# Kernel tuning notes

Measured on AMD Instinct MI355X. Metric: run time of the kernel, lower is better.

Reference implementation:

```python
import jax, jax.numpy as jnp
import numpy as np

NUM_CLASSES = 81
THRESH_HI = 0.5
THRESH_LO = 0.4
GAMMA = 2.0
ALPHA = 0.25
VARIANCE = (0.1, 0.2)  # cfg['variance'] in ssd.pytorch
B, P, T = 32, 24564, 20


def setup_inputs() -> dict:
    key = jax.random.key(0)
    k1, k2, k3, k4, k5, k6, k7 = jax.random.split(key, 7)
    loc_data = jax.random.normal(k1, (B, P, 4), jnp.float32)
    conf_data = jax.random.normal(k2, (B, P, NUM_CLASSES), jnp.float32)
    # priors in center form (cx, cy, w, h), all in [0,1]
    pcxy = jax.random.uniform(k3, (P, 2), minval=0.05, maxval=0.95)
    pwh = jax.random.uniform(k4, (P, 2), minval=0.04, maxval=0.5)
    priors = jnp.concatenate([pcxy, pwh], axis=-1).astype(jnp.float32)
    # ground-truth boxes in point form (xmin, ymin, xmax, ymax) + label
    tcxy = jax.random.uniform(k5, (B, T, 2), minval=0.1, maxval=0.9)
    twh = jax.random.uniform(k6, (B, T, 2), minval=0.05, maxval=0.4)
    boxes = jnp.clip(jnp.concatenate([tcxy - twh / 2, tcxy + twh / 2], -1), 0.0, 1.0)
    labels = jax.random.randint(k7, (B, T), 0, NUM_CLASSES - 1).astype(jnp.float32)
    targets = jnp.concatenate([boxes, labels[..., None]], axis=-1)  # [B,T,5]
    return {"loc_data": loc_data, "conf_data": conf_data, "priors": priors, "targets": targets}


def point_form(pr):
    # center form -> (xmin,ymin,xmax,ymax)
    return jnp.concatenate([pr[:, :2] - pr[:, 2:] / 2, pr[:, :2] + pr[:, 2:] / 2], -1)


def jaccard(box_a, box_b):
    # box_a [T,4], box_b [P,4], both point form -> IoU [T,P]
    lt = jnp.maximum(box_a[:, None, :2], box_b[None, :, :2])
    rb = jnp.minimum(box_a[:, None, 2:], box_b[None, :, 2:])
    wh = jnp.clip(rb - lt, 0.0)
    inter = wh[..., 0] * wh[..., 1]
    area_a = ((box_a[:, 2] - box_a[:, 0]) * (box_a[:, 3] - box_a[:, 1]))[:, None]
    area_b = ((box_b[:, 2] - box_b[:, 0]) * (box_b[:, 3] - box_b[:, 1]))[None, :]
    return inter / (area_a + area_b - inter)


def encode(matched, priors):
    # matched [P,4] point form, priors [P,4] center form
    g_cxcy = ((matched[:, :2] + matched[:, 2:]) / 2 - priors[:, :2]) / (VARIANCE[0] * priors[:, 2:])
    g_wh = jnp.log((matched[:, 2:] - matched[:, :2]) / priors[:, 2:]) / VARIANCE[1]
    return jnp.concatenate([g_cxcy, g_wh], -1)


def match_one(truths, labels, priors):
    # truths [T,4] point form, labels [T], priors [P,4] center form
    ov = jaccard(truths, point_form(priors))          # [T,P]
    best_prior_idx = jnp.argmax(ov, axis=1)           # [T] best prior per gt
    best_truth_overlap = jnp.max(ov, axis=0)          # [P]
    best_truth_idx = jnp.argmax(ov, axis=0)           # [P]
    # ensure every gt box keeps its best prior
    best_truth_overlap = best_truth_overlap.at[best_prior_idx].set(2.0)
    best_truth_idx = best_truth_idx.at[best_prior_idx].set(jnp.arange(truths.shape[0]))
    matched = truths[best_truth_idx]                  # [P,4]
    conf = labels[best_truth_idx].astype(jnp.int32) + 1
    conf = jnp.where(best_truth_overlap < THRESH_HI, -1, conf)  # ignore band
    conf = jnp.where(best_truth_overlap < THRESH_LO, 0, conf)   # background
    return encode(matched, priors), conf


def reference(loc_data, conf_data, priors, targets):
    truths = targets[..., :4]
    labels = targets[..., 4]
    loc_t, conf_t = jax.vmap(lambda t, l: match_one(t, l, priors))(truths, labels)
    pos = conf_t > 0                                  # [B,P]
    # smooth L1 over positive priors (sum reduction)
    diff = loc_data - loc_t
    ad = jnp.abs(diff)
    sl1 = jnp.where(ad < 1.0, 0.5 * diff * diff, ad - 0.5)
    loss_l = jnp.sum(sl1 * pos[..., None])
    # focal loss over ALL locations (ignore conf==-1)
    logits = conf_data.reshape(-1, NUM_CLASSES)
    tgt = conf_t.reshape(-1)
    valid = tgt >= 0
    tgt_safe = jnp.where(valid, tgt, 0)
    logpt = jnp.take_along_axis(jax.nn.log_softmax(logits, -1), tgt_safe[:, None], 1)[:, 0]
    pt = jnp.exp(logpt)
    alpha_t = jnp.where(tgt > 0, ALPHA, 1.0 - ALPHA)
    fl = -alpha_t * (1.0 - pt) ** GAMMA * logpt
    loss_c = jnp.sum(jnp.where(valid, fl, 0.0))
    n = jnp.sum(pos).astype(loc_data.dtype)
    return loss_l / n, loss_c / n
```

## Files before the change

### kernel.cpp

```cpp
#include <hip/hip_runtime.h>

#define NCLS 81
#define BB 32
#define PP 24564
#define TT 20
#define BP_SEGS 8
#define BP_SEG 3072
#define NBLK 1024
#define NWAVES (NBLK * 4)
#define WC_TOTAL ((BB * PP) / 8)

#define GLOAD_LDS16(g, l)                                                  \
    __builtin_amdgcn_global_load_lds(                                      \
        (const __attribute__((address_space(1))) void*)(g),                \
        (__attribute__((address_space(3))) void*)(l), 16, 0, 0)

__global__ __launch_bounds__(1024)
void k_bp(const float* __restrict__ priors,
          const float* __restrict__ targets,
          unsigned long long* __restrict__ bp_final,
          unsigned long long* __restrict__ bovbt)
{
    const int seg = blockIdx.x;
    const int b = blockIdx.y;

    __shared__ float trb[TT * 5];
    __shared__ unsigned long long wred[TT][16];
    if (threadIdx.x < TT * 5) trb[threadIdx.x] = targets[b * TT * 5 + threadIdx.x];
    __syncthreads();

    float X1[3], Y1[3], X2[3], Y2[3], pa[3];
    unsigned int pkey[3];
    bool ok[3];
    #pragma unroll
    for (int j = 0; j < 3; ++j) {
        int p = seg * BP_SEG + j * 1024 + threadIdx.x;
        ok[j] = p < PP;
        float4 pr = ok[j] ? ((const float4*)priors)[p] : make_float4(1.f, 1.f, 0.f, 0.f);
        float hw = __fmul_rn(pr.z, 0.5f), hh = __fmul_rn(pr.w, 0.5f);
        X1[j] = __fsub_rn(pr.x, hw); Y1[j] = __fsub_rn(pr.y, hh);
        X2[j] = __fadd_rn(pr.x, hw); Y2[j] = __fadd_rn(pr.y, hh);
        pa[j] = __fmul_rn(__fsub_rn(X2[j], X1[j]), __fsub_rn(Y2[j], Y1[j]));
        pkey[j] = 0xFFFFFFFFu - (unsigned)p;
    }

    const int wv = threadIdx.x >> 6;
    const int lane = threadIdx.x & 63;

    unsigned long long bkey[3] = {0ull, 0ull, 0ull};

    for (int t = 0; t < TT; ++t) {
        float tx1 = trb[t * 5 + 0], ty1 = trb[t * 5 + 1];
        float tx2 = trb[t * 5 + 2], ty2 = trb[t * 5 + 3];
        float ta = __fmul_rn(__fsub_rn(tx2, tx1), __fsub_rn(ty2, ty1));

        unsigned long long best = 0ull;
        #pragma unroll
        for (int j = 0; j < 3; ++j) {
            float lx = fmaxf(tx1, X1[j]), ly = fmaxf(ty1, Y1[j]);
            float rx = fminf(tx2, X2[j]), ry = fminf(ty2, Y2[j]);
            float w = fmaxf(__fsub_rn(rx, lx), 0.0f);
            float h = fmaxf(__fsub_rn(ry, ly), 0.0f);
            float inter = __fmul_rn(w, h);
            float denom = __fsub_rn(__fadd_rn(ta, pa[j]), inter);
            float ov = __fdiv_rn(inter, denom);
            unsigned long long ovhi = (unsigned long long)__float_as_uint(ov) << 32;
            unsigned long long key = ok[j] ? (ovhi | pkey[j]) : 0ull;
            if (key > best) best = key;
            unsigned long long rowk = ovhi | (unsigned long long)(31 - t);
            if (rowk > bkey[j]) bkey[j] = rowk;
        }
        #pragma unroll
        for (int s = 32; s; s >>= 1) {
            unsigned long long o = __shfl_xor(best, s, 64);
            if (o > best) best = o;
        }
        if (lane == 0) wred[t][wv] = best;
    }

    #pragma unroll
    for (int j = 0; j < 3; ++j) {
        int p = seg * BP_SEG + j * 1024 + threadIdx.x;
        if (p < PP) bovbt[b * PP + p] = bkey[j];
    }

    __syncthreads();
    if (threadIdx.x < TT) {
        unsigned long long m = wred[threadIdx.x][0];
        #pragma unroll
        for (int w = 1; w < 16; ++w) if (wred[threadIdx.x][w] > m) m = wred[threadIdx.x][w];
        atomicMax(&bp_final[b * TT + threadIdx.x], m);
    }
}

__global__ __launch_bounds__(256, 4)
void k_stream(const float* __restrict__ conf,
              const float* __restrict__ loc,
              const float* __restrict__ priors,
              const float* __restrict__ targets,
              const unsigned long long* __restrict__ bp_final,
              const unsigned long long* __restrict__ bovbt,
              float* __restrict__ pl, float* __restrict__ pn, float* __restrict__ pc)
{
    __shared__ float buf[4][2][8 * NCLS];
    __shared__ float trbAll[BB * TT * 5];
    __shared__ unsigned int bpAll[BB * TT];
    __shared__ float red[256];

    const int tid = threadIdx.x;
    const int wv = tid >> 6;
    const int lane = tid & 63;
    const int rloc = lane >> 3;
    const int k = lane & 7;
    const float4* conf4 = (const float4*)conf;

    for (int i = tid; i < BB * TT * 5; i += 256) trbAll[i] = targets[i];
    for (int i = tid; i < BB * TT; i += 256)
        bpAll[i] = 0xFFFFFFFFu - (unsigned)(bp_final[i] & 0xFFFFFFFFull);
    __syncthreads();

    auto stage = [&](int wc, int bi) {
        const float4* src = conf4 + (size_t)wc * 162;
        float4* dst = (float4*)(&buf[wv][bi][0]);
        GLOAD_LDS16(src + lane, dst + lane);
        GLOAD_LDS16(src + 64 + lane, dst + 64 + lane);
        if (lane < 34) GLOAD_LDS16(src + 128 + lane, dst + 128 + lane);
    };

    const int gw = blockIdx.x * 4 + wv;
    float accL = 0.0f, accN = 0.0f, accC = 0.0f;

    int wc = gw;
    int cur = 0;
    unsigned long long rk = 0ull;
    float4 pr4 = make_float4(0.f, 0.f, 1.f, 1.f);
    float4 ld4 = make_float4(0.f, 0.f, 0.f, 0.f);
    {
        stage(wc, 0);
        int r0 = wc * 8 + rloc;
        int b0 = r0 / PP;
        int p0 = r0 - b0 * PP;
        if (k == 0) {
            rk = bovbt[r0];
            pr4 = *(const float4*)(priors + p0 * 4);
            ld4 = *(const float4*)(loc + (size_t)r0 * 4);
        }
    }

    for (; wc < WC_TOTAL; wc += NWAVES) {
        const int wn = wc + NWAVES;
        const bool hasnext = wn < WC_TOTAL;
        unsigned long long rkn = 0ull;
        float4 pr4n = pr4, ld4n = ld4;
        if (hasnext) {
            stage(wn, cur ^ 1);
            int rn = wn * 8 + rloc;
            int bn = rn / PP;
            int pn_ = rn - bn * PP;
            if (k == 0) {
                rkn = bovbt[rn];
                pr4n = *(const float4*)(priors + pn_ * 4);
                ld4n = *(const float4*)(loc + (size_t)rn * 4);
            }
        }
        __builtin_amdgcn_sched_barrier(0);
        if (hasnext) asm volatile("s_waitcnt vmcnt(6)" ::: "memory");
        else         asm volatile("s_waitcnt vmcnt(0)" ::: "memory");
        __builtin_amdgcn_sched_barrier(0);

        const float* row = &buf[wv][cur][0] + rloc * NCLS;
        float se = 0.0f;
        #pragma unroll
        for (int i = 0; i < 10; ++i) se += __expf(row[k * 10 + i]);
        if (k == 0) se += __expf(row[80]);
        se += __shfl_xor(se, 1, 8);
        se += __shfl_xor(se, 2, 8);
        se += __shfl_xor(se, 4, 8);

        const int r = wc * 8 + rloc;
        const int b = r / PP;
        const int p = r - b * PP;
        const unsigned int* bpb = &bpAll[b * TT];
        const float* trb = &trbAll[b * TT * 5];

        int t0 = (k < 4) ? 3 * k : 12 + 2 * (k - 4);
        int nt = (k < 4) ? 3 : 2;
        int ft = -1;
        #pragma unroll
        for (int u = 0; u < 3; ++u) {
            if (u < nt) {
                int t = t0 + u;
                if (bpb[t] == (unsigned)p) ft = t;
            }
        }
        #pragma unroll
        for (int s = 4; s; s >>= 1) {
            int of = __shfl_xor(ft, s, 8);
            if (of > ft) ft = of;
        }

        if (k == 0) {
            int bt;
            float bov;
            if (ft >= 0) { bt = ft; bov = 2.0f; }
            else {
                bt = 31 - (int)(rk & 31ull);
                bov = __uint_as_float((unsigned)(rk >> 32));
            }
            int cc = (int)trb[bt * 5 + 4] + 1;
            if (bov < 0.5f) cc = -1;
            if (bov < 0.4f) cc = 0;

            if (cc > 0) {
                float mx1 = trb[bt * 5 + 0], my1 = trb[bt * 5 + 1];
                float mx2 = trb[bt * 5 + 2], my2 = trb[bt * 5 + 3];
                float cx = __fmul_rn(__fadd_rn(mx1, mx2), 0.5f);
                float cy = __fmul_rn(__fadd_rn(my1, my2), 0.5f);
                float gx = __fdiv_rn(__fsub_rn(cx, pr4.x), __fmul_rn(0.1f, pr4.z));
                float gy = __fdiv_rn(__fsub_rn(cy, pr4.y), __fmul_rn(0.1f, pr4.w));
                float gw_ = __fdiv_rn(logf(__fdiv_rn(__fsub_rn(mx2, mx1), pr4.z)), 0.2f);
                float gh_ = __fdiv_rn(logf(__fdiv_rn(__fsub_rn(my2, my1), pr4.w)), 0.2f);
                float g0 = ld4.x - gx, g1 = ld4.y - gy, g2 = ld4.z - gw_, g3 = ld4.w - gh_;
                float a0 = fabsf(g0), a1 = fabsf(g1), a2 = fabsf(g2), a3 = fabsf(g3);
                accL += (a0 < 1.0f) ? 0.5f * g0 * g0 : (a0 - 0.5f);
                accL += (a1 < 1.0f) ? 0.5f * g1 * g1 : (a1 - 0.5f);
                accL += (a2 < 1.0f) ? 0.5f * g2 * g2 : (a2 - 0.5f);
                accL += (a3 < 1.0f) ? 0.5f * g3 * g3 : (a3 - 0.5f);
                accN += 1.0f;
            }
            if (cc >= 0) {
                float xt = row[cc];
                float logpt = xt - __logf(se);
                float pt = __expf(logpt);
                float at = (cc > 0) ? 0.25f : 0.75f;
                float om = 1.0f - pt;
                accC -= at * om * om * logpt;
            }
        }
        rk = rkn; pr4 = pr4n; ld4 = ld4n;
        cur ^= 1;
    }

    __syncthreads();
    red[tid] = accL;
    __syncthreads();
    for (int s = 128; s; s >>= 1) {
        if (tid < s) red[tid] += red[tid + s];
        __syncthreads();
    }
    if (tid == 0) pl[blockIdx.x] = red[0];
    __syncthreads();

    red[tid] = accN;
    __syncthreads();
    for (int s = 128; s; s >>= 1) {
        if (tid < s) red[tid] += red[tid + s];
        __syncthreads();
    }
    if (tid == 0) pn[blockIdx.x] = red[0];
    __syncthreads();

    red[tid] = accC;
    __syncthreads();
    for (int s = 128; s; s >>= 1) {
        if (tid < s) red[tid] += red[tid + s];
        __syncthreads();
    }
    if (tid == 0) pc[blockIdx.x] = red[0];
}

__global__ __launch_bounds__(256)
void k_final(const float* __restrict__ pl, const float* __restrict__ pn,
             const float* __restrict__ pc, float* __restrict__ out)
{
    __shared__ float sl[256], sc[256], sn[256];
    float L = 0.0f, C = 0.0f, N = 0.0f;
    for (int i = threadIdx.x; i < NBLK; i += 256) {
        L += pl[i]; N += pn[i]; C += pc[i];
    }
    sl[threadIdx.x] = L; sc[threadIdx.x] = C; sn[threadIdx.x] = N;
    __syncthreads();
    for (int s = 128; s; s >>= 1) {
        if (threadIdx.x < s) {
            sl[threadIdx.x] += sl[threadIdx.x + s];
            sc[threadIdx.x] += sc[threadIdx.x + s];
            sn[threadIdx.x] += sn[threadIdx.x + s];
        }
        __syncthreads();
    }
    if (threadIdx.x == 0) {
        out[0] = sl[0] / sn[0];
        out[1] = sc[0] / sn[0];
    }
}

extern "C" void kernel_launch(void* const* d_in, const int* in_sizes, int n_in,
                              void* d_out, int out_size, void* d_ws, size_t ws_size,
                              hipStream_t stream)
{
    const float* loc     = (const float*)d_in[0];
    const float* conf    = (const float*)d_in[1];
    const float* priors  = (const float*)d_in[2];
    const float* targets = (const float*)d_in[3];
    float* out = (float*)d_out;

    char* ws = (char*)d_ws;
    unsigned long long* bp_final = (unsigned long long*)ws;
    unsigned long long* bovbt    = (unsigned long long*)(ws + 65536);
    float* pl = (float*)(ws + 65536 + 6291456);
    float* pn = pl + NBLK;
    float* pc = pn + NBLK;

    hipMemsetAsync(bp_final, 0, BB * TT * sizeof(unsigned long long), stream);
    k_bp<<<dim3(BP_SEGS, BB), 1024, 0, stream>>>(priors, targets, bp_final, bovbt);
    k_stream<<<NBLK, 256, 0, stream>>>(conf, loc, priors, targets, bp_final,
                                       bovbt, pl, pn, pc);
    k_final<<<1, 256, 0, stream>>>(pl, pn, pc, out);
}
```

Before: 89.25 us.

## Replace LDS-staged wave streaming with per-thread four-row direct float4 loads

The streaming kernel drops the double-buffered global-to-LDS staging, where eight lanes shared each row. Each thread now reads four consecutive 81-class rows (81 float4s) straight from global memory, does the logsumexp itself, and runs the matching tail for each row. The grid becomes one pass of 768 blocks with no grid-stride loop, and priors and loc are loaded only for positive rows. The risk is poor coalescing, since each thread walks a 1296-byte stride, plus more register pressure and no explicit latency hiding.

```diff
diff --git a/kernel.cpp b/kernel.cpp
--- a/kernel.cpp
+++ b/kernel.cpp
@@ -6,14 +6,8 @@
 #define TT 20
 #define BP_SEGS 8
 #define BP_SEG 3072
-#define NBLK 1024
-#define NWAVES (NBLK * 4)
-#define WC_TOTAL ((BB * PP) / 8)
-
-#define GLOAD_LDS16(g, l)                                                  \
-    __builtin_amdgcn_global_load_lds(                                      \
-        (const __attribute__((address_space(1))) void*)(g),                \
-        (__attribute__((address_space(3))) void*)(l), 16, 0, 0)
+#define NG ((BB * PP) / 4)
+#define NSBLK 768
 
 __global__ __launch_bounds__(1024)
 void k_bp(const float* __restrict__ priors,
@@ -93,113 +87,72 @@
     }
 }
 
-__global__ __launch_bounds__(256, 4)
+__global__ __launch_bounds__(256)
 void k_stream(const float* __restrict__ conf,
               const float* __restrict__ loc,
               const float* __restrict__ priors,
+              const unsigned long long* __restrict__ bovbt,
               const float* __restrict__ targets,
               const unsigned long long* __restrict__ bp_final,
-              const unsigned long long* __restrict__ bovbt,
               float* __restrict__ pl, float* __restrict__ pn, float* __restrict__ pc)
 {
-    __shared__ float buf[4][2][8 * NCLS];
     __shared__ float trbAll[BB * TT * 5];
     __shared__ unsigned int bpAll[BB * TT];
     __shared__ float red[256];
 
     const int tid = threadIdx.x;
-    const int wv = tid >> 6;
-    const int lane = tid & 63;
-    const int rloc = lane >> 3;
-    const int k = lane & 7;
-    const float4* conf4 = (const float4*)conf;
-
     for (int i = tid; i < BB * TT * 5; i += 256) trbAll[i] = targets[i];
     for (int i = tid; i < BB * TT; i += 256)
         bpAll[i] = 0xFFFFFFFFu - (unsigned)(bp_final[i] & 0xFFFFFFFFull);
     __syncthreads();
 
-    auto stage = [&](int wc, int bi) {
-        const float4* src = conf4 + (size_t)wc * 162;
-        float4* dst = (float4*)(&buf[wv][bi][0]);
-        GLOAD_LDS16(src + lane, dst + lane);
-        GLOAD_LDS16(src + 64 + lane, dst + 64 + lane);
-        if (lane < 34) GLOAD_LDS16(src + 128 + lane, dst + 128 + lane);
-    };
-
-    const int gw = blockIdx.x * 4 + wv;
     float accL = 0.0f, accN = 0.0f, accC = 0.0f;
 
-    int wc = gw;
-    int cur = 0;
-    unsigned long long rk = 0ull;
-    float4 pr4 = make_float4(0.f, 0.f, 1.f, 1.f);
-    float4 ld4 = make_float4(0.f, 0.f, 0.f, 0.f);
-    {
-        stage(wc, 0);
-        int r0 = wc * 8 + rloc;
-        int b0 = r0 / PP;
-        int p0 = r0 - b0 * PP;
-        if (k == 0) {
-            rk = bovbt[r0];
-            pr4 = *(const float4*)(priors + p0 * 4);
-            ld4 = *(const float4*)(loc + (size_t)r0 * 4);
-        }
-    }
-
-    for (; wc < WC_TOTAL; wc += NWAVES) {
-        const int wn = wc + NWAVES;
-        const bool hasnext = wn < WC_TOTAL;
-        unsigned long long rkn = 0ull;
-        float4 pr4n = pr4, ld4n = ld4;
-        if (hasnext) {
-            stage(wn, cur ^ 1);
-            int rn = wn * 8 + rloc;
-            int bn = rn / PP;
-            int pn_ = rn - bn * PP;
-            if (k == 0) {
-                rkn = bovbt[rn];
-                pr4n = *(const float4*)(priors + pn_ * 4);
-                ld4n = *(const float4*)(loc + (size_t)rn * 4);
-            }
-        }
-        __builtin_amdgcn_sched_barrier(0);
-        if (hasnext) asm volatile("s_waitcnt vmcnt(6)" ::: "memory");
-        else         asm volatile("s_waitcnt vmcnt(0)" ::: "memory");
-        __builtin_amdgcn_sched_barrier(0);
-
-        const float* row = &buf[wv][cur][0] + rloc * NCLS;
-        float se = 0.0f;
-        #pragma unroll
-        for (int i = 0; i < 10; ++i) se += __expf(row[k * 10 + i]);
-        if (k == 0) se += __expf(row[80]);
-        se += __shfl_xor(se, 1, 8);
-        se += __shfl_xor(se, 2, 8);
-        se += __shfl_xor(se, 4, 8);
-
-        const int r = wc * 8 + rloc;
-        const int b = r / PP;
-        const int p = r - b * PP;
-        const unsigned int* bpb = &bpAll[b * TT];
-        const float* trb = &trbAll[b * TT * 5];
-
-        int t0 = (k < 4) ? 3 * k : 12 + 2 * (k - 4);
-        int nt = (k < 4) ? 3 : 2;
-        int ft = -1;
-        #pragma unroll
-        for (int u = 0; u < 3; ++u) {
-            if (u < nt) {
-                int t = t0 + u;
+    const int grp = blockIdx.x * 256 + tid;
+    if (grp < NG) {
+        const float4* g4 = (const float4*)conf + (size_t)grp * 81;
+
+        float4 vb0 = g4[20], vb1 = g4[40], vb2 = g4[60];
+        float se0 = 0.0f, se1 = 0.0f, se2 = 0.0f, se3 = 0.0f;
+        #pragma unroll
+        for (int j = 0; j < 20; ++j) {
+            float4 v = g4[j];
+            se0 += __expf(v.x) + __expf(v.y) + __expf(v.z) + __expf(v.w);
+        }
+        se0 += __expf(vb0.x);
+        se1 = __expf(vb0.y) + __expf(vb0.z) + __expf(vb0.w);
+        #pragma unroll
+        for (int j = 21; j < 40; ++j) {
+            float4 v = g4[j];
+            se1 += __expf(v.x) + __expf(v.y) + __expf(v.z) + __expf(v.w);
+        }
+        se1 += __expf(vb1.x) + __expf(vb1.y);
+        se2 = __expf(vb1.z) + __expf(vb1.w);
+        #pragma unroll
+        for (int j = 41; j < 60; ++j) {
+            float4 v = g4[j];
+            se2 += __expf(v.x) + __expf(v.y) + __expf(v.z) + __expf(v.w);
+        }
+        se2 += __expf(vb2.x) + __expf(vb2.y) + __expf(vb2.z);
+        se3 = __expf(vb2.w);
+        #pragma unroll
+        for (int j = 61; j < 81; ++j) {
+            float4 v = g4[j];
+            se3 += __expf(v.x) + __expf(v.y) + __expf(v.z) + __expf(v.w);
+        }
+
+        auto tail = [&](int r, float se) {
+            int b = r / PP;
+            int p = r - b * PP;
+            const float* trb = &trbAll[b * TT * 5];
+            const unsigned int* bpb = &bpAll[b * TT];
+
+            unsigned long long rk = bovbt[r];
+            int ft = -1;
+            #pragma unroll
+            for (int t = 0; t < TT; ++t) {
                 if (bpb[t] == (unsigned)p) ft = t;
             }
-        }
-        #pragma unroll
-        for (int s = 4; s; s >>= 1) {
-            int of = __shfl_xor(ft, s, 8);
-            if (of > ft) ft = of;
-        }
-
-        if (k == 0) {
             int bt;
             float bov;
             if (ft >= 0) { bt = ft; bov = 2.0f; }
@@ -212,15 +165,17 @@
             if (bov < 0.4f) cc = 0;
 
             if (cc > 0) {
+                float4 pr = *(const float4*)(priors + p * 4);
                 float mx1 = trb[bt * 5 + 0], my1 = trb[bt * 5 + 1];
                 float mx2 = trb[bt * 5 + 2], my2 = trb[bt * 5 + 3];
                 float cx = __fmul_rn(__fadd_rn(mx1, mx2), 0.5f);
                 float cy = __fmul_rn(__fadd_rn(my1, my2), 0.5f);
-                float gx = __fdiv_rn(__fsub_rn(cx, pr4.x), __fmul_rn(0.1f, pr4.z));
-                float gy = __fdiv_rn(__fsub_rn(cy, pr4.y), __fmul_rn(0.1f, pr4.w));
-                float gw_ = __fdiv_rn(logf(__fdiv_rn(__fsub_rn(mx2, mx1), pr4.z)), 0.2f);
-                float gh_ = __fdiv_rn(logf(__fdiv_rn(__fsub_rn(my2, my1), pr4.w)), 0.2f);
-                float g0 = ld4.x - gx, g1 = ld4.y - gy, g2 = ld4.z - gw_, g3 = ld4.w - gh_;
+                float gx = __fdiv_rn(__fsub_rn(cx, pr.x), __fmul_rn(0.1f, pr.z));
+                float gy = __fdiv_rn(__fsub_rn(cy, pr.y), __fmul_rn(0.1f, pr.w));
+                float gw = __fdiv_rn(logf(__fdiv_rn(__fsub_rn(mx2, mx1), pr.z)), 0.2f);
+                float gh = __fdiv_rn(logf(__fdiv_rn(__fsub_rn(my2, my1), pr.w)), 0.2f);
+                float4 ld = *(const float4*)(loc + (size_t)r * 4);
+                float g0 = ld.x - gx, g1 = ld.y - gy, g2 = ld.z - gw, g3 = ld.w - gh;
                 float a0 = fabsf(g0), a1 = fabsf(g1), a2 = fabsf(g2), a3 = fabsf(g3);
                 accL += (a0 < 1.0f) ? 0.5f * g0 * g0 : (a0 - 0.5f);
                 accL += (a1 < 1.0f) ? 0.5f * g1 * g1 : (a1 - 0.5f);
@@ -229,19 +184,20 @@
                 accN += 1.0f;
             }
             if (cc >= 0) {
-                float xt = row[cc];
+                float xt = conf[(size_t)r * NCLS + cc];
                 float logpt = xt - __logf(se);
                 float pt = __expf(logpt);
                 float at = (cc > 0) ? 0.25f : 0.75f;
                 float om = 1.0f - pt;
                 accC -= at * om * om * logpt;
             }
-        }
-        rk = rkn; pr4 = pr4n; ld4 = ld4n;
-        cur ^= 1;
-    }
-
-    __syncthreads();
+        };
+        tail(grp * 4 + 0, se0);
+        tail(grp * 4 + 1, se1);
+        tail(grp * 4 + 2, se2);
+        tail(grp * 4 + 3, se3);
+    }
+
     red[tid] = accL;
     __syncthreads();
     for (int s = 128; s; s >>= 1) {
@@ -275,7 +231,7 @@
 {
     __shared__ float sl[256], sc[256], sn[256];
     float L = 0.0f, C = 0.0f, N = 0.0f;
-    for (int i = threadIdx.x; i < NBLK; i += 256) {
+    for (int i = threadIdx.x; i < NSBLK; i += 256) {
         L += pl[i]; N += pn[i]; C += pc[i];
     }
     sl[threadIdx.x] = L; sc[threadIdx.x] = C; sn[threadIdx.x] = N;
@@ -308,12 +264,12 @@
     unsigned long long* bp_final = (unsigned long long*)ws;
     unsigned long long* bovbt    = (unsigned long long*)(ws + 65536);
     float* pl = (float*)(ws + 65536 + 6291456);
-    float* pn = pl + NBLK;
-    float* pc = pn + NBLK;
+    float* pn = pl + NSBLK;
+    float* pc = pn + NSBLK;
 
     hipMemsetAsync(bp_final, 0, BB * TT * sizeof(unsigned long long), stream);
     k_bp<<<dim3(BP_SEGS, BB), 1024, 0, stream>>>(priors, targets, bp_final, bovbt);
-    k_stream<<<NBLK, 256, 0, stream>>>(conf, loc, priors, targets, bp_final,
-                                       bovbt, pl, pn, pc);
+    k_stream<<<NSBLK, 256, 0, stream>>>(conf, loc, priors, bovbt, targets, bp_final,
+                                        pl, pn, pc);
     k_final<<<1, 256, 0, stream>>>(pl, pn, pc, out);
 }
```

Result: slower. 125.0 us (+40.1%).
